# Kernel optimization log

Hardware: AMD Instinct MI355X
Metric: run time of the kernel (lower is better)

Reference implementation:

```python
import jax, jax.numpy as jnp
import numpy as np

NEG_SLOPE = 0.2  # PyG GATConv default leaky_relu slope


def gat_conv(x, src, dst, n, W, a_src, a_dst, bias, concat):
    """PyG-style GATConv (add_self_loops already applied to src/dst)."""
    H, C = a_src.shape
    h = (x @ W).reshape(n, H, C)                      # [N,H,C]
    al_src = jnp.einsum('nhc,hc->nh', h, a_src)       # [N,H]
    al_dst = jnp.einsum('nhc,hc->nh', h, a_dst)       # [N,H]
    e = jax.nn.leaky_relu(al_src[src] + al_dst[dst], NEG_SLOPE)  # [E,H]
    # segment softmax over incoming edges of each dst node
    m = jax.ops.segment_max(e, dst, num_segments=n)   # [N,H]
    ex = jnp.exp(e - m[dst])
    denom = jax.ops.segment_sum(ex, dst, num_segments=n)
    alpha = ex / denom[dst]                            # [E,H]
    out = jax.ops.segment_sum(h[src] * alpha[:, :, None], dst, num_segments=n)  # [N,H,C]
    if concat:
        out = out.reshape(n, H * C)
    else:
        out = out.mean(axis=1)
    return out + bias


def setup_inputs() -> dict:
    key = jax.random.key(0)
    ks = jax.random.split(key, 12)
    N, E = 100000, 1600000
    IN, HID, OUT, H = 128, 16, 32, 4
    x = jax.random.normal(ks[0], (N, IN), dtype=jnp.float32)
    edge_index = jax.random.randint(ks[1], (2, E), 0, N, dtype=jnp.int64)
    s = 0.1
    W1 = jax.random.normal(ks[2], (IN, H * HID), dtype=jnp.float32) * s
    a_src1 = jax.random.normal(ks[3], (H, HID), dtype=jnp.float32) * s
    a_dst1 = jax.random.normal(ks[4], (H, HID), dtype=jnp.float32) * s
    b1 = jnp.zeros((H * HID,), dtype=jnp.float32)
    W2 = jax.random.normal(ks[5], (H * HID, H * OUT), dtype=jnp.float32) * s
    a_src2 = jax.random.normal(ks[6], (H, OUT), dtype=jnp.float32) * s
    a_dst2 = jax.random.normal(ks[7], (H, OUT), dtype=jnp.float32) * s
    b2 = jnp.zeros((OUT,), dtype=jnp.float32)
    return {"x": x, "edge_index": edge_index,
            "W1": W1, "a_src1": a_src1, "a_dst1": a_dst1, "b1": b1,
            "W2": W2, "a_src2": a_src2, "a_dst2": a_dst2, "b2": b2}


def reference(x, edge_index, W1, a_src1, a_dst1, b1, W2, a_src2, a_dst2, b2):
    n = x.shape[0]
    loop = jnp.arange(n, dtype=edge_index.dtype)
    src = jnp.concatenate([edge_index[0], loop])
    dst = jnp.concatenate([edge_index[1], loop])
    # dropout is identity at inference
    h = gat_conv(x, src, dst, n, W1, a_src1, a_dst1, b1, concat=True)
    h = gat_conv(h, src, dst, n, W2, a_src2, a_dst2, b2, concat=False)
    h = jax.nn.elu(h)
    return jax.nn.log_softmax(h, axis=1)
```

## Files before the change

### kernel.cpp

```cpp
#include <hip/hip_runtime.h>
#include <hip/hip_fp16.h>
#include <cstdint>
#include <cstddef>

#define NEG 0.2f
#define TILE 4096
#define WEXP(e) __expf((e) > 0.f ? (e) : NEG * (e))

typedef int i4v __attribute__((ext_vector_type(4)));

__device__ __forceinline__ i4v ld_i4(const int* p) {
    i4v r;
    __builtin_memcpy(&r, p, 16);
    return r;
}
__device__ __forceinline__ __half2 bch(unsigned v) { __half2 r; *(unsigned*)&r = v; return r; }
__device__ __forceinline__ __half2 bchi(int v) { __half2 r; *(int*)&r = v; return r; }


__global__ __launch_bounds__(256) void bhist_k(const int* __restrict__ ei, int* __restrict__ bc, int E, int nbk) {
    __shared__ int sb[256];
    int t = threadIdx.x;
    sb[t] = 0;
    __syncthreads();
    int stride = gridDim.x * 256;
    for (int i = blockIdx.x * 256 + t; i < E; i += stride) {
        int d = __builtin_nontemporal_load(ei + E + i);
        atomicAdd(&sb[d >> 9], 1);
    }
    __syncthreads();
    if (t < nbk && sb[t] > 0) atomicAdd(&bc[t], sb[t]);
}


__global__ __launch_bounds__(256) void bscan_k(const int* __restrict__ bc, int* __restrict__ bb,
                                               int* __restrict__ curA, int nbk) {
    __shared__ int sm[256];
    int t = threadIdx.x;
    int v = (t < nbk) ? bc[t] : 0;
    sm[t] = v; __syncthreads();
    for (int off = 1; off < 256; off <<= 1) {
        int u = (t >= off) ? sm[t - off] : 0;
        __syncthreads();
        sm[t] += u;
        __syncthreads();
    }
    if (t < nbk) {
        int ex = sm[t] - v;
        bb[t] = ex;
        curA[t] = ex;
        if (t == nbk - 1) bb[nbk] = sm[t];
    }
}


__global__ __launch_bounds__(256) void partA_k(const int* __restrict__ ei, int* __restrict__ curA,
                                               uint2* __restrict__ pairs, int E, int nbk) {
    __shared__ int scnt[256];
    __shared__ int sc[256];
    __shared__ int sbase[256];
    __shared__ int gbase[256];
    __shared__ int cur2[256];
    __shared__ int ssrc[TILE];
    __shared__ int sdst[TILE];
    int t = threadIdx.x;
    int ntiles = (E + TILE - 1) / TILE;
    for (int tile = blockIdx.x; tile < ntiles; tile += gridDim.x) {
        int base = tile * TILE;
        int cntE = min(TILE, E - base);
        scnt[t] = 0;
        __syncthreads();
        int mys[16], myd[16];
        #pragma unroll
        for (int j = 0; j < 16; j++) {
            int i = base + t + 256 * j;
            int s = 0, d = -1;
            if (i < E) {
                s = __builtin_nontemporal_load(ei + i);
                d = __builtin_nontemporal_load(ei + E + i);
            }
            mys[j] = s; myd[j] = d;
            if (d >= 0) atomicAdd(&scnt[d >> 9], 1);
        }
        __syncthreads();
        sc[t] = scnt[t];
        __syncthreads();
        for (int off = 1; off < 256; off <<= 1) {
            int u = (t >= off) ? sc[t - off] : 0;
            __syncthreads();
            sc[t] += u;
            __syncthreads();
        }
        int myb = sc[t] - scnt[t];
        sbase[t] = myb;
        cur2[t] = myb;
        if (t < nbk && scnt[t] > 0) gbase[t] = atomicAdd(&curA[t], scnt[t]);
        __syncthreads();
        #pragma unroll
        for (int j = 0; j < 16; j++) {
            int d = myd[j];
            if (d >= 0) {
                int b = d >> 9;
                int pos = atomicAdd(&cur2[b], 1);
                ssrc[pos] = mys[j];
                sdst[pos] = d;
            }
        }
        __syncthreads();
        for (int i = t; i < cntE; i += 256) {
            int d = sdst[i];
            int b = d >> 9;
            int addr = gbase[b] + (i - sbase[b]);
            pairs[addr] = make_uint2((unsigned)ssrc[i], (unsigned)d);
        }
        __syncthreads();
    }
}


__global__ __launch_bounds__(256) void partB2_k(const uint2* __restrict__ pin, const int* __restrict__ bb,
                                                int* __restrict__ rp, int* __restrict__ cnt,
                                                int* __restrict__ srcout, int N) {
    __shared__ int cur[512];
    __shared__ int sc[512];
    int b = blockIdx.x, t = threadIdx.x;
    int d0 = b << 9;
    cur[t] = 0; cur[t + 256] = 0;
    __syncthreads();
    int ebase = bb[b], eend = bb[b + 1];
    for (int j = ebase + t; j < eend; j += 256) {
        int d = (int)pin[j].y;
        atomicAdd(&cur[d - d0], 1);
    }
    __syncthreads();
    sc[t] = cur[t]; sc[t + 256] = cur[t + 256];
    __syncthreads();
    for (int off = 1; off <= 256; off <<= 1) {
        int a0 = (t >= off) ? sc[t - off] : 0;
        int a1 = sc[t + 256 - off];
        __syncthreads();
        sc[t] += a0; sc[t + 256] += a1;
        __syncthreads();
    }
    int base0 = ebase + sc[t] - cur[t];
    int base1 = ebase + sc[t + 256] - cur[t + 256];
    if (d0 + t < N)       { rp[d0 + t] = base0;       cnt[d0 + t] = cur[t]; }
    if (d0 + t + 256 < N) { rp[d0 + t + 256] = base1; cnt[d0 + t + 256] = cur[t + 256]; }
    cur[t] = base0; cur[t + 256] = base1;
    __syncthreads();
    for (int j = ebase + t; j < eend; j += 256) {
        uint2 p = pin[j];
        int d = (int)p.y;
        int pos = atomicAdd(&cur[d - d0], 1);
        srcout[pos] = (int)p.x;
    }
}


__global__ __launch_bounds__(256) void gemm1_k(const float* __restrict__ x, const float* __restrict__ W,
                                               const float* __restrict__ a_src, const float* __restrict__ a_dst,
                                               __half* __restrict__ h, float* __restrict__ alsrc,
                                               float* __restrict__ aldst, int N) {
    __shared__ float Bs[128 * 64];
    __shared__ float xt[64 * 68];
    int t = threadIdx.x;
    for (int i = t; i < 128 * 64 / 4; i += 256)
        ((float4*)Bs)[i] = ((const float4*)W)[i];
    int ct = t & 15, rt = t >> 4;
    int head = ct >> 2, cq = ct & 3;
    float asv[4], adv[4];
    #pragma unroll
    for (int j = 0; j < 4; j++) {
        asv[j] = a_src[head * 16 + 4 * cq + j];
        adv[j] = a_dst[head * 16 + 4 * cq + j];
    }
    int ntiles = (N + 63) >> 6;
    for (int tile = blockIdx.x; tile < ntiles; tile += gridDim.x) {
        int r0 = tile << 6;
        float acc[4][4];
        #pragma unroll
        for (int i = 0; i < 4; i++)
            #pragma unroll
            for (int j = 0; j < 4; j++) acc[i][j] = 0.f;
        for (int kc = 0; kc < 128; kc += 64) {
            __syncthreads();
            int srow = t >> 4, sf4 = t & 15;
            #pragma unroll
            for (int p = 0; p < 4; p++) {
                int r = r0 + srow + 16 * p;
                float4 v = make_float4(0.f, 0.f, 0.f, 0.f);
                if (r < N) v = *(const float4*)(x + (size_t)r * 128 + kc + 4 * sf4);
                int rr = srow + 16 * p, k0 = 4 * sf4;
                int colb = 4 * (((rr >> 2) + sf4) & 15) + (rr & 3);
                xt[(k0 + 0) * 68 + colb] = v.x;
                xt[(k0 + 1) * 68 + colb] = v.y;
                xt[(k0 + 2) * 68 + colb] = v.z;
                xt[(k0 + 3) * 68 + colb] = v.w;
            }
            __syncthreads();
            #pragma unroll 4
            for (int k = 0; k < 64; k++) {
                float4 bv = *(float4*)&Bs[(kc + k) * 64 + 4 * ct];
                float4 xv = *(float4*)&xt[k * 68 + 4 * ((rt + (k >> 2)) & 15)];
                acc[0][0] = fmaf(xv.x, bv.x, acc[0][0]);
                acc[0][1] = fmaf(xv.x, bv.y, acc[0][1]);
                acc[0][2] = fmaf(xv.x, bv.z, acc[0][2]);
                acc[0][3] = fmaf(xv.x, bv.w, acc[0][3]);
                acc[1][0] = fmaf(xv.y, bv.x, acc[1][0]);
                acc[1][1] = fmaf(xv.y, bv.y, acc[1][1]);
                acc[1][2] = fmaf(xv.y, bv.z, acc[1][2]);
                acc[1][3] = fmaf(xv.y, bv.w, acc[1][3]);
                acc[2][0] = fmaf(xv.z, bv.x, acc[2][0]);
                acc[2][1] = fmaf(xv.z, bv.y, acc[2][1]);
                acc[2][2] = fmaf(xv.z, bv.z, acc[2][2]);
                acc[2][3] = fmaf(xv.z, bv.w, acc[2][3]);
                acc[3][0] = fmaf(xv.w, bv.x, acc[3][0]);
                acc[3][1] = fmaf(xv.w, bv.y, acc[3][1]);
                acc[3][2] = fmaf(xv.w, bv.z, acc[3][2]);
                acc[3][3] = fmaf(xv.w, bv.w, acc[3][3]);
            }
        }
        #pragma unroll
        for (int i = 0; i < 4; i++) {
            int r = r0 + 4 * rt + i;
            float ps = 0.f, pd = 0.f;
            #pragma unroll
            for (int j = 0; j < 4; j++) {
                ps = fmaf(acc[i][j], asv[j], ps);
                pd = fmaf(acc[i][j], adv[j], pd);
            }
            ps += __shfl_xor(ps, 1); ps += __shfl_xor(ps, 2);
            pd += __shfl_xor(pd, 1); pd += __shfl_xor(pd, 2);
            if (r < N) {
                __half2 h0 = __floats2half2_rn(acc[i][0], acc[i][1]);
                __half2 h1 = __floats2half2_rn(acc[i][2], acc[i][3]);
                *(__half2*)(h + (size_t)r * 64 + 4 * ct) = h0;
                *(__half2*)(h + (size_t)r * 64 + 4 * ct + 2) = h1;
                if (cq == 0) { alsrc[r * 4 + head] = ps; aldst[r * 4 + head] = pd; }
            }
        }
    }
}


__global__ __launch_bounds__(256) void prew_k(const float* __restrict__ W2, const float* __restrict__ as2,
                                              const float* __restrict__ ad2, float* __restrict__ was,
                                              float* __restrict__ wad, uint2* __restrict__ wkg) {
    int t = threadIdx.x;
    int k = t >> 2, hh = t & 3;
    const float* wrow = W2 + k * 128 + hh * 32;
    const float* av = as2 + hh * 32;
    const float* dv = ad2 + hh * 32;
    float s = 0.f, ds = 0.f;
    #pragma unroll 8
    for (int c = 0; c < 32; c++) {
        float w = wrow[c];
        s = fmaf(w, av[c], s);
        ds = fmaf(w, dv[c], ds);
    }
    was[t] = s;
    wad[t] = ds;
    #pragma unroll
    for (int j = 0; j < 8; j++) {
        int e = t * 8 + j;
        int cp = e >> 7, k2 = e & 127;
        int h = k2 >> 5, kk = (2 * k2) & 63;
        const float* w0 = W2 + kk * 128 + h * 32;
        const float* w1 = W2 + (kk + 1) * 128 + h * 32;
        __half2 hx = __floats2half2_rn(w0[2 * cp], w1[2 * cp]);
        __half2 hy = __floats2half2_rn(w0[2 * cp + 1], w1[2 * cp + 1]);
        uint2 v;
        v.x = *(unsigned*)&hx;
        v.y = *(unsigned*)&hy;
        wkg[e] = v;
    }
}


__global__ __launch_bounds__(256) void node1_k(const __half* __restrict__ h, const int* __restrict__ srccol,
                                               const float* __restrict__ alsrc, const float* __restrict__ aldst,
                                               const int* __restrict__ rp, const int* __restrict__ cnt,
                                               const float* __restrict__ bias,
                                               const float* __restrict__ was, const float* __restrict__ wad,
                                               __half* __restrict__ out,
                                               float* __restrict__ alsrc2, float* __restrict__ aldst2, int N) {
    int t = threadIdx.x;
    int d = (blockIdx.x * 256 + t) >> 4;
    if (d >= N) return;
    int c = t & 15;
    int eh = c >> 2, hh = c & 3;
    int mh = c >> 2;
    const uint2* hb = (const uint2*)h;
    float myad = aldst[d * 4 + hh];
    float selfw = WEXP(alsrc[d * 4 + hh] + myad);
    __half2 sh2 = __float2half2_rn(selfw);
    int si = *(int*)&sh2;
    float mden = (eh == 0) ? selfw : 0.f;
    uint2 u = hb[((size_t)d << 4) + c];
    __half2 smy = bchi(__shfl(si, mh, 16));
    __half2 acc0 = __hmul2(smy, bch(u.x));
    __half2 acc1 = __hmul2(smy, bch(u.y));
    int start = rp[d], deg = cnt[d];
    int nq = deg >> 2;
    int i = 0;
    #define N1_PROC(G0, G1, G2, G3, AW) { \
        float w_ = WEXP((AW) + myad); \
        mden += w_; \
        __half2 wh_ = __float2half2_rn(w_); \
        int wi_ = *(int*)&wh_; \
        __half2 q0_ = bchi(__shfl(wi_, 0 + mh, 16)); \
        __half2 q1_ = bchi(__shfl(wi_, 4 + mh, 16)); \
        __half2 q2_ = bchi(__shfl(wi_, 8 + mh, 16)); \
        __half2 q3_ = bchi(__shfl(wi_, 12 + mh, 16)); \
        acc0 = __hfma2(q0_, bch(G0.x), acc0); acc1 = __hfma2(q0_, bch(G0.y), acc1); \
        acc0 = __hfma2(q1_, bch(G1.x), acc0); acc1 = __hfma2(q1_, bch(G1.y), acc1); \
        acc0 = __hfma2(q2_, bch(G2.x), acc0); acc1 = __hfma2(q2_, bch(G2.y), acc1); \
        acc0 = __hfma2(q3_, bch(G3.x), acc0); acc1 = __hfma2(q3_, bch(G3.y), acc1); }
    if (nq > 0) {
        i4v sv = ld_i4(srccol + start);
        uint2 g0 = hb[((size_t)(unsigned)sv.x << 4) + c];
        uint2 g1 = hb[((size_t)(unsigned)sv.y << 4) + c];
        uint2 g2 = hb[((size_t)(unsigned)sv.z << 4) + c];
        uint2 g3 = hb[((size_t)(unsigned)sv.w << 4) + c];
        int my = (eh == 0) ? sv.x : (eh == 1) ? sv.y : (eh == 2) ? sv.z : sv.w;
        float aw = alsrc[(size_t)my * 4 + hh];
        i4v nv = (nq > 1) ? ld_i4(srccol + start + 4) : sv;
        for (int q = 1; q < nq; q++) {
            uint2 n0 = hb[((size_t)(unsigned)nv.x << 4) + c];
            uint2 n1 = hb[((size_t)(unsigned)nv.y << 4) + c];
            uint2 n2 = hb[((size_t)(unsigned)nv.z << 4) + c];
            uint2 n3 = hb[((size_t)(unsigned)nv.w << 4) + c];
            int nmy = (eh == 0) ? nv.x : (eh == 1) ? nv.y : (eh == 2) ? nv.z : nv.w;
            float naw = alsrc[(size_t)nmy * 4 + hh];
            i4v nv2 = (q + 1 < nq) ? ld_i4(srccol + start + 4 * (q + 1)) : nv;
            N1_PROC(g0, g1, g2, g3, aw)
            g0 = n0; g1 = n1; g2 = n2; g3 = n3; aw = naw; nv = nv2;
        }
        N1_PROC(g0, g1, g2, g3, aw)
        i = nq << 2;
    }
    for (; i < deg; i++) {
        int s = srccol[start + i];
        uint2 us = hb[((size_t)(unsigned)s << 4) + c];
        float w = WEXP(alsrc[(size_t)s * 4 + hh] + myad);
        mden += (eh == 0) ? w : 0.f;
        __half2 wh = __float2half2_rn(w);
        int wi = *(int*)&wh;
        __half2 qq = bchi(__shfl(wi, mh, 16));
        acc0 = __hfma2(qq, bch(us.x), acc0);
        acc1 = __hfma2(qq, bch(us.y), acc1);
    }
    mden += __shfl_xor(mden, 4, 16);
    mden += __shfl_xor(mden, 8, 16);
    float den = __shfl(mden, mh, 16);
    float inv = 1.f / den;
    float2 f0 = __half22float2(acc0), f1 = __half22float2(acc1);
    float4 b = *(const float4*)(bias + 4 * c);
    float v0 = f0.x * inv + b.x, v1 = f0.y * inv + b.y;
    float v2 = f1.x * inv + b.z, v3 = f1.y * inv + b.w;
    __half2 o0 = __floats2half2_rn(v0, v1);
    __half2 o1 = __floats2half2_rn(v2, v3);
    uint2 o; o.x = *(unsigned*)&o0; o.y = *(unsigned*)&o1;
    *(uint2*)(out + (size_t)d * 64 + 4 * c) = o;
    const float4* was4 = (const float4*)was;
    const float4* wad4 = (const float4*)wad;
    float4 wa0 = was4[4 * c + 0], wa1 = was4[4 * c + 1], wa2 = was4[4 * c + 2], wa3 = was4[4 * c + 3];
    float4 wd0 = wad4[4 * c + 0], wd1 = wad4[4 * c + 1], wd2 = wad4[4 * c + 2], wd3 = wad4[4 * c + 3];
    float4 ps, pd;
    ps.x = fmaf(v0, wa0.x, fmaf(v1, wa1.x, fmaf(v2, wa2.x, v3 * wa3.x)));
    ps.y = fmaf(v0, wa0.y, fmaf(v1, wa1.y, fmaf(v2, wa2.y, v3 * wa3.y)));
    ps.z = fmaf(v0, wa0.z, fmaf(v1, wa1.z, fmaf(v2, wa2.z, v3 * wa3.z)));
    ps.w = fmaf(v0, wa0.w, fmaf(v1, wa1.w, fmaf(v2, wa2.w, v3 * wa3.w)));
    pd.x = fmaf(v0, wd0.x, fmaf(v1, wd1.x, fmaf(v2, wd2.x, v3 * wd3.x)));
    pd.y = fmaf(v0, wd0.y, fmaf(v1, wd1.y, fmaf(v2, wd2.y, v3 * wd3.y)));
    pd.z = fmaf(v0, wd0.z, fmaf(v1, wd1.z, fmaf(v2, wd2.z, v3 * wd3.z)));
    pd.w = fmaf(v0, wd0.w, fmaf(v1, wd1.w, fmaf(v2, wd2.w, v3 * wd3.w)));
    #pragma unroll
    for (int off = 1; off <= 8; off <<= 1) {
        ps.x += __shfl_xor(ps.x, off); ps.y += __shfl_xor(ps.y, off);
        ps.z += __shfl_xor(ps.z, off); ps.w += __shfl_xor(ps.w, off);
        pd.x += __shfl_xor(pd.x, off); pd.y += __shfl_xor(pd.y, off);
        pd.z += __shfl_xor(pd.z, off); pd.w += __shfl_xor(pd.w, off);
    }
    if (c == 0) {
        *(float4*)(alsrc2 + (size_t)d * 4) = ps;
        *(float4*)(aldst2 + (size_t)d * 4) = pd;
    }
}


#define EDGE_SH(J, U) { \
    __half2 l_ = bch(U.x), h_ = bch(U.y); \
    __half2 qa = bchi(__shfl(wi, 4 * J + 0, 16)); \
    __half2 qb = bchi(__shfl(wi, 4 * J + 1, 16)); \
    __half2 qc = bchi(__shfl(wi, 4 * J + 2, 16)); \
    __half2 qd = bchi(__shfl(wi, 4 * J + 3, 16)); \
    aA0 = __hfma2(qa, l_, aA0); aA1 = __hfma2(qa, h_, aA1); \
    aB0 = __hfma2(qb, l_, aB0); aB1 = __hfma2(qb, h_, aB1); \
    aC0 = __hfma2(qc, l_, aC0); aC1 = __hfma2(qc, h_, aC1); \
    aD0 = __hfma2(qd, l_, aD0); aD1 = __hfma2(qd, h_, aD1); }

__global__ __launch_bounds__(256) void node2_k(const __half* __restrict__ h1o, const int* __restrict__ srccol,
                                               const float* __restrict__ alsrc, const float* __restrict__ aldst,
                                               const int* __restrict__ rp, const int* __restrict__ cnt,
                                               const uint2* __restrict__ wkg, const float* __restrict__ b2,
                                               float* __restrict__ out, int N) {
    __shared__ unsigned wt[16 * 260];
    __shared__ unsigned ys[16 * 132];
    int t = threadIdx.x;
    #pragma unroll
    for (int j = 0; j < 8; j++) {
        int i = t + 256 * j;
        int cp0 = i >> 7, k20 = i & 127;
        *(uint2*)&wt[cp0 * 260 + 2 * k20] = wkg[i];
    }
    int d = blockIdx.x * 16 + (t >> 4);
    int c = t & 15;
    bool live = d < N;
    __half2 hz = __float2half2_rn(0.f);
    __half2 y00 = hz, y01 = hz, y10 = hz, y11 = hz;
    __half2 y20 = hz, y21 = hz, y30 = hz, y31 = hz;
    if (live) {
        int eh = c >> 2;
        int hh = c & 3;
        const uint2* hb = (const uint2*)h1o;
        float myad = aldst[d * 4 + hh];
        float selfw = WEXP(alsrc[d * 4 + hh] + myad);
        __half2 selfh = __float2half2_rn(selfw);
        int selfi = *(int*)&selfh;
        float mden = (eh == 0) ? selfw : 0.f;
        uint2 u = hb[((size_t)d << 4) + c];
        __half2 lo = bch(u.x), hi = bch(u.y);
        __half2 sA = bchi(__shfl(selfi, 0, 16));
        __half2 sB = bchi(__shfl(selfi, 1, 16));
        __half2 sC = bchi(__shfl(selfi, 2, 16));
        __half2 sD = bchi(__shfl(selfi, 3, 16));
        __half2 aA0 = __hmul2(sA, lo), aA1 = __hmul2(sA, hi);
        __half2 aB0 = __hmul2(sB, lo), aB1 = __hmul2(sB, hi);
        __half2 aC0 = __hmul2(sC, lo), aC1 = __hmul2(sC, hi);
        __half2 aD0 = __hmul2(sD, lo), aD1 = __hmul2(sD, hi);
        int start = rp[d], deg = cnt[d];
        int nq = deg >> 2;
        int i = 0;
        #define N2_PROC(G0, G1, G2, G3, AW) { \
            float w_ = WEXP((AW) + myad); \
            mden += w_; \
            __half2 wh_ = __float2half2_rn(w_); \
            int wi = *(int*)&wh_; \
            EDGE_SH(0, G0) EDGE_SH(1, G1) EDGE_SH(2, G2) EDGE_SH(3, G3) }
        if (nq > 0) {
            i4v sv = ld_i4(srccol + start);
            uint2 g0 = hb[((size_t)(unsigned)sv.x << 4) + c];
            uint2 g1 = hb[((size_t)(unsigned)sv.y << 4) + c];
            uint2 g2 = hb[((size_t)(unsigned)sv.z << 4) + c];
            uint2 g3 = hb[((size_t)(unsigned)sv.w << 4) + c];
            int my = (eh == 0) ? sv.x : (eh == 1) ? sv.y : (eh == 2) ? sv.z : sv.w;
            float aw = alsrc[(size_t)my * 4 + hh];
            i4v nv = (nq > 1) ? ld_i4(srccol + start + 4) : sv;
            for (int q = 1; q < nq; q++) {
                uint2 n0 = hb[((size_t)(unsigned)nv.x << 4) + c];
                uint2 n1 = hb[((size_t)(unsigned)nv.y << 4) + c];
                uint2 n2 = hb[((size_t)(unsigned)nv.z << 4) + c];
                uint2 n3 = hb[((size_t)(unsigned)nv.w << 4) + c];
                int nmy = (eh == 0) ? nv.x : (eh == 1) ? nv.y : (eh == 2) ? nv.z : nv.w;
                float naw = alsrc[(size_t)nmy * 4 + hh];
                i4v nv2 = (q + 1 < nq) ? ld_i4(srccol + start + 4 * (q + 1)) : nv;
                N2_PROC(g0, g1, g2, g3, aw)
                g0 = n0; g1 = n1; g2 = n2; g3 = n3; aw = naw; nv = nv2;
            }
            N2_PROC(g0, g1, g2, g3, aw)
            i = nq << 2;
        }
        for (; i < deg; i++) {
            int s = srccol[start + i];
            uint2 us = hb[((size_t)(unsigned)s << 4) + c];
            float w = WEXP(alsrc[(size_t)s * 4 + hh] + myad);
            mden += (eh == 0) ? w : 0.f;
            __half2 wh = __float2half2_rn(w);
            int wi = *(int*)&wh;
            EDGE_SH(0, us)
        }
        mden += __shfl_xor(mden, 4, 16);
        mden += __shfl_xor(mden, 8, 16);
        float dnA = __shfl(mden, 0, 16);
        float dnB = __shfl(mden, 1, 16);
        float dnC = __shfl(mden, 2, 16);
        float dnD = __shfl(mden, 3, 16);
        __half2 jA = __float2half2_rn(0.25f / dnA), jB = __float2half2_rn(0.25f / dnB);
        __half2 jC = __float2half2_rn(0.25f / dnC), jD = __float2half2_rn(0.25f / dnD);
        y00 = __hmul2(jA, aA0); y01 = __hmul2(jA, aA1);
        y10 = __hmul2(jB, aB0); y11 = __hmul2(jB, aB1);
        y20 = __hmul2(jC, aC0); y21 = __hmul2(jC, aC1);
        y30 = __hmul2(jD, aD0); y31 = __hmul2(jD, aD1);
        unsigned* yp = ys + (t >> 4) * 132 + 2 * c;
        *(uint2*)&yp[0]  = make_uint2(*(unsigned*)&y00, *(unsigned*)&y01);
        *(uint2*)&yp[32] = make_uint2(*(unsigned*)&y10, *(unsigned*)&y11);
        *(uint2*)&yp[64] = make_uint2(*(unsigned*)&y20, *(unsigned*)&y21);
        *(uint2*)&yp[96] = make_uint2(*(unsigned*)&y30, *(unsigned*)&y31);
    }
    __syncthreads();
    if (!live) return;
    int n = t >> 4, cp = c;
    const unsigned* yr = ys + n * 132;
    const unsigned* wr = wt + cp * 260;
    float f0 = 0.f, f1 = 0.f;
    for (int kc = 0; kc < 128; kc += 16) {
        __half2 a0 = hz, a1 = hz;
        #pragma unroll
        for (int j = 0; j < 4; j++) {
            int k2 = kc + 4 * j;
            uint4 yv = *(const uint4*)&yr[k2];
            uint4 w0 = *(const uint4*)&wr[2 * k2];
            uint4 w1 = *(const uint4*)&wr[2 * k2 + 4];
            a0 = __hfma2(bch(yv.x), bch(w0.x), a0); a1 = __hfma2(bch(yv.x), bch(w0.y), a1);
            a0 = __hfma2(bch(yv.y), bch(w0.z), a0); a1 = __hfma2(bch(yv.y), bch(w0.w), a1);
            a0 = __hfma2(bch(yv.z), bch(w1.x), a0); a1 = __hfma2(bch(yv.z), bch(w1.y), a1);
            a0 = __hfma2(bch(yv.w), bch(w1.z), a0); a1 = __hfma2(bch(yv.w), bch(w1.w), a1);
        }
        float2 q0 = __half22float2(a0), q1 = __half22float2(a1);
        f0 += q0.x + q0.y;
        f1 += q1.x + q1.y;
    }
    float e0 = f0 + b2[2 * cp];
    float e1 = f1 + b2[2 * cp + 1];
    e0 = e0 > 0.f ? e0 : __expf(e0) - 1.f;
    e1 = e1 > 0.f ? e1 : __expf(e1) - 1.f;
    float mx = fmaxf(e0, e1);
    #pragma unroll
    for (int off = 1; off <= 8; off <<= 1) mx = fmaxf(mx, __shfl_xor(mx, off, 16));
    float sm = __expf(e0 - mx) + __expf(e1 - mx);
    #pragma unroll
    for (int off = 1; off <= 8; off <<= 1) sm += __shfl_xor(sm, off, 16);
    float ls = mx + __logf(sm);
    float2 ov = make_float2(e0 - ls, e1 - ls);
    *(float2*)(out + (size_t)d * 32 + 2 * cp) = ov;
}


extern "C" void kernel_launch(void* const* d_in, const int* in_sizes, int n_in,
                              void* d_out, int out_size, void* d_ws, size_t ws_size,
                              hipStream_t stream) {
    const float* x   = (const float*)d_in[0];
    const int*   ei  = (const int*)d_in[1];
    const float* W1  = (const float*)d_in[2];
    const float* as1 = (const float*)d_in[3];
    const float* ad1 = (const float*)d_in[4];
    const float* b1  = (const float*)d_in[5];
    const float* W2  = (const float*)d_in[6];
    const float* as2 = (const float*)d_in[7];
    const float* ad2 = (const float*)d_in[8];
    const float* b2  = (const float*)d_in[9];
    float* out = (float*)d_out;
    int N = in_sizes[0] / 128;
    int E = in_sizes[1] / 2;

    char* base = (char*)d_ws;
    size_t off = 0;
    auto alloc = [&](size_t bytes) -> char* {
        char* p = base + off;
        off = (off + bytes + 255) & ~(size_t)255;
        return p;
    };
    __half* h1h   = (__half*)alloc((size_t)N * 64 * 2);
    __half* h1o   = (__half*)alloc((size_t)N * 64 * 2);
    uint2*  pairs = (uint2*)alloc((size_t)E * 8);
    float* alsrc1 = (float*)alloc((size_t)N * 4 * 4);
    float* aldst1 = (float*)alloc((size_t)N * 4 * 4);
    float* alsrc2 = (float*)alloc((size_t)N * 4 * 4);
    float* aldst2 = (float*)alloc((size_t)N * 4 * 4);
    float* was    = (float*)alloc(256 * 4);
    float* wad    = (float*)alloc(256 * 4);
    uint2* wkg    = (uint2*)alloc(2048 * 8);
    int* cnt  = (int*)alloc((size_t)N * 4);
    int* rp   = (int*)alloc((size_t)N * 4);
    int* curA = (int*)alloc(256 * 4);
    int* bc   = (int*)alloc(256 * 4);
    int* bb   = (int*)alloc(260 * 4);
    int* srccol = (int*)alloc((size_t)E * 4);

    int nbk = (N + 511) >> 9;
    int ntilesA = (E + TILE - 1) / TILE;
    int nt1 = (N + 63) >> 6;

    prew_k<<<1, 256, 0, stream>>>(W2, as2, ad2, was, wad, wkg);
    hipMemsetAsync(bc, 0, 256 * 4, stream);
    bhist_k<<<512, 256, 0, stream>>>(ei, bc, E, nbk);
    bscan_k<<<1, 256, 0, stream>>>(bc, bb, curA, nbk);
    partA_k<<<ntilesA, 256, 0, stream>>>(ei, curA, pairs, E, nbk);
    partB2_k<<<nbk, 256, 0, stream>>>(pairs, bb, rp, cnt, srccol, N);

    gemm1_k<<<(nt1 + 1) / 2, 256, 0, stream>>>(x, W1, as1, ad1, h1h, alsrc1, aldst1, N);
    node1_k<<<(N + 15) / 16, 256, 0, stream>>>(h1h, srccol, alsrc1, aldst1, rp, cnt, b1,
                                               was, wad, h1o, alsrc2, aldst2, N);
    node2_k<<<(N + 15) / 16, 256, 0, stream>>>(h1o, srccol, alsrc2, aldst2, rp, cnt,
                                               wkg, b2, out, N);
}
```

Before: 312.3 us.

## Use packed half FMA in layer-1 GEMM and register-block node2 projection

The layer-1 feature GEMM now converts W and x tiles to packed half2 in shared memory and accumulates with __hfma2 in 16-step chunks, flushing to fp32. This halves shared-memory footprint and doubles math throughput per instruction, at the cost of reduced precision in the x@W product. In node2, the output projection now has half the threads each compute two nodes, so each weight load from shared memory is reused across both rows.

```diff
diff --git a/kernel.cpp b/kernel.cpp
--- a/kernel.cpp
+++ b/kernel.cpp
@@ -161,11 +161,14 @@
                                                const float* __restrict__ a_src, const float* __restrict__ a_dst,
                                                __half* __restrict__ h, float* __restrict__ alsrc,
                                                float* __restrict__ aldst, int N) {
-    __shared__ float Bs[128 * 64];
-    __shared__ float xt[64 * 68];
+    __shared__ unsigned wh[64 * 64];
+    __shared__ unsigned xh[64 * 68];
     int t = threadIdx.x;
-    for (int i = t; i < 128 * 64 / 4; i += 256)
-        ((float4*)Bs)[i] = ((const float4*)W)[i];
+    for (int i = t; i < 4096; i += 256) {
+        int k2 = i >> 6, col = i & 63;
+        __half2 hv = __floats2half2_rn(W[(2 * k2) * 64 + col], W[(2 * k2 + 1) * 64 + col]);
+        wh[i] = *(unsigned*)&hv;
+    }
     int ct = t & 15, rt = t >> 4;
     int head = ct >> 2, cq = ct & 3;
     float asv[4], adv[4];
@@ -177,48 +180,55 @@
     int ntiles = (N + 63) >> 6;
     for (int tile = blockIdx.x; tile < ntiles; tile += gridDim.x) {
         int r0 = tile << 6;
+        __syncthreads();
+        #pragma unroll
+        for (int p = 0; p < 8; p++) {
+            int i = t + 256 * p;
+            int f4i = i & 31, row = i >> 5;
+            int r = r0 + row;
+            float4 v = make_float4(0.f, 0.f, 0.f, 0.f);
+            if (r < N) v = *(const float4*)(x + (size_t)r * 128 + 4 * f4i);
+            __half2 p0 = __floats2half2_rn(v.x, v.y);
+            __half2 p1 = __floats2half2_rn(v.z, v.w);
+            xh[(2 * f4i) * 68 + row] = *(unsigned*)&p0;
+            xh[(2 * f4i + 1) * 68 + row] = *(unsigned*)&p1;
+        }
+        __syncthreads();
         float acc[4][4];
         #pragma unroll
         for (int i = 0; i < 4; i++)
             #pragma unroll
             for (int j = 0; j < 4; j++) acc[i][j] = 0.f;
-        for (int kc = 0; kc < 128; kc += 64) {
-            __syncthreads();
-            int srow = t >> 4, sf4 = t & 15;
+        __half2 hz = __float2half2_rn(0.f);
+        for (int kc = 0; kc < 64; kc += 16) {
+            __half2 ah[4][4];
             #pragma unroll
-            for (int p = 0; p < 4; p++) {
-                int r = r0 + srow + 16 * p;
-                float4 v = make_float4(0.f, 0.f, 0.f, 0.f);
-                if (r < N) v = *(const float4*)(x + (size_t)r * 128 + kc + 4 * sf4);
-                int rr = srow + 16 * p, k0 = 4 * sf4;
-                int colb = 4 * (((rr >> 2) + sf4) & 15) + (rr & 3);
-                xt[(k0 + 0) * 68 + colb] = v.x;
-                xt[(k0 + 1) * 68 + colb] = v.y;
-                xt[(k0 + 2) * 68 + colb] = v.z;
-                xt[(k0 + 3) * 68 + colb] = v.w;
+            for (int i = 0; i < 4; i++)
+                #pragma unroll
+                for (int j = 0; j < 4; j++) ah[i][j] = hz;
+            #pragma unroll
+            for (int j = 0; j < 16; j++) {
+                int k2 = kc + j;
+                uint4 wv = *(const uint4*)&wh[k2 * 64 + 4 * ct];
+                uint4 xv = *(const uint4*)&xh[k2 * 68 + 4 * rt];
+                __half2 w0 = bch(wv.x), w1 = bch(wv.y), w2 = bch(wv.z), w3 = bch(wv.w);
+                __half2 x0 = bch(xv.x), x1 = bch(xv.y), x2 = bch(xv.z), x3 = bch(xv.w);
+                ah[0][0] = __hfma2(x0, w0, ah[0][0]); ah[0][1] = __hfma2(x0, w1, ah[0][1]);
+                ah[0][2] = __hfma2(x0, w2, ah[0][2]); ah[0][3] = __hfma2(x0, w3, ah[0][3]);
+                ah[1][0] = __hfma2(x1, w0, ah[1][0]); ah[1][1] = __hfma2(x1, w1, ah[1][1]);
+                ah[1][2] = __hfma2(x1, w2, ah[1][2]); ah[1][3] = __hfma2(x1, w3, ah[1][3]);
+                ah[2][0] = __hfma2(x2, w0, ah[2][0]); ah[2][1] = __hfma2(x2, w1, ah[2][1]);
+                ah[2][2] = __hfma2(x2, w2, ah[2][2]); ah[2][3] = __hfma2(x2, w3, ah[2][3]);
+                ah[3][0] = __hfma2(x3, w0, ah[3][0]); ah[3][1] = __hfma2(x3, w1, ah[3][1]);
+                ah[3][2] = __hfma2(x3, w2, ah[3][2]); ah[3][3] = __hfma2(x3, w3, ah[3][3]);
             }
-            __syncthreads();
-            #pragma unroll 4
-            for (int k = 0; k < 64; k++) {
-                float4 bv = *(float4*)&Bs[(kc + k) * 64 + 4 * ct];
-                float4 xv = *(float4*)&xt[k * 68 + 4 * ((rt + (k >> 2)) & 15)];
-                acc[0][0] = fmaf(xv.x, bv.x, acc[0][0]);
-                acc[0][1] = fmaf(xv.x, bv.y, acc[0][1]);
-                acc[0][2] = fmaf(xv.x, bv.z, acc[0][2]);
-                acc[0][3] = fmaf(xv.x, bv.w, acc[0][3]);
-                acc[1][0] = fmaf(xv.y, bv.x, acc[1][0]);
-                acc[1][1] = fmaf(xv.y, bv.y, acc[1][1]);
-                acc[1][2] = fmaf(xv.y, bv.z, acc[1][2]);
-                acc[1][3] = fmaf(xv.y, bv.w, acc[1][3]);
-                acc[2][0] = fmaf(xv.z, bv.x, acc[2][0]);
-                acc[2][1] = fmaf(xv.z, bv.y, acc[2][1]);
-                acc[2][2] = fmaf(xv.z, bv.z, acc[2][2]);
-                acc[2][3] = fmaf(xv.z, bv.w, acc[2][3]);
-                acc[3][0] = fmaf(xv.w, bv.x, acc[3][0]);
-                acc[3][1] = fmaf(xv.w, bv.y, acc[3][1]);
-                acc[3][2] = fmaf(xv.w, bv.z, acc[3][2]);
-                acc[3][3] = fmaf(xv.w, bv.w, acc[3][3]);
-            }
+            #pragma unroll
+            for (int i = 0; i < 4; i++)
+                #pragma unroll
+                for (int j = 0; j < 4; j++) {
+                    float2 q = __half22float2(ah[i][j]);
+                    acc[i][j] += q.x + q.y;
+                }
         }
         #pragma unroll
         for (int i = 0; i < 4; i++) {
@@ -418,8 +428,6 @@
     int c = t & 15;
     bool live = d < N;
     __half2 hz = __float2half2_rn(0.f);
-    __half2 y00 = hz, y01 = hz, y10 = hz, y11 = hz;
-    __half2 y20 = hz, y21 = hz, y30 = hz, y31 = hz;
     if (live) {
         int eh = c >> 2;
         int hh = c & 3;
@@ -488,10 +496,10 @@
         float dnD = __shfl(mden, 3, 16);
         __half2 jA = __float2half2_rn(0.25f / dnA), jB = __float2half2_rn(0.25f / dnB);
         __half2 jC = __float2half2_rn(0.25f / dnC), jD = __float2half2_rn(0.25f / dnD);
-        y00 = __hmul2(jA, aA0); y01 = __hmul2(jA, aA1);
-        y10 = __hmul2(jB, aB0); y11 = __hmul2(jB, aB1);
-        y20 = __hmul2(jC, aC0); y21 = __hmul2(jC, aC1);
-        y30 = __hmul2(jD, aD0); y31 = __hmul2(jD, aD1);
+        __half2 y00 = __hmul2(jA, aA0), y01 = __hmul2(jA, aA1);
+        __half2 y10 = __hmul2(jB, aB0), y11 = __hmul2(jB, aB1);
+        __half2 y20 = __hmul2(jC, aC0), y21 = __hmul2(jC, aC1);
+        __half2 y30 = __hmul2(jD, aD0), y31 = __hmul2(jD, aD1);
         unsigned* yp = ys + (t >> 4) * 132 + 2 * c;
         *(uint2*)&yp[0]  = make_uint2(*(unsigned*)&y00, *(unsigned*)&y01);
         *(uint2*)&yp[32] = make_uint2(*(unsigned*)&y10, *(unsigned*)&y11);
@@ -499,41 +507,63 @@
         *(uint2*)&yp[96] = make_uint2(*(unsigned*)&y30, *(unsigned*)&y31);
     }
     __syncthreads();
-    if (!live) return;
-    int n = t >> 4, cp = c;
-    const unsigned* yr = ys + n * 132;
+    if (t >= 128) return;
+    int np = t >> 4, cp = t & 15;
+    int d0 = blockIdx.x * 16 + 2 * np;
+    if (d0 >= N) return;
+    bool l1 = (d0 + 1) < N;
+    const unsigned* yr0 = ys + (2 * np) * 132;
+    const unsigned* yr1 = yr0 + 132;
     const unsigned* wr = wt + cp * 260;
-    float f0 = 0.f, f1 = 0.f;
+    float f00 = 0.f, f01 = 0.f, f10 = 0.f, f11 = 0.f;
     for (int kc = 0; kc < 128; kc += 16) {
-        __half2 a0 = hz, a1 = hz;
+        __half2 a00 = hz, a01 = hz, a10 = hz, a11 = hz;
         #pragma unroll
         for (int j = 0; j < 4; j++) {
             int k2 = kc + 4 * j;
-            uint4 yv = *(const uint4*)&yr[k2];
+            uint4 yv0 = *(const uint4*)&yr0[k2];
+            uint4 yv1 = *(const uint4*)&yr1[k2];
             uint4 w0 = *(const uint4*)&wr[2 * k2];
             uint4 w1 = *(const uint4*)&wr[2 * k2 + 4];
-            a0 = __hfma2(bch(yv.x), bch(w0.x), a0); a1 = __hfma2(bch(yv.x), bch(w0.y), a1);
-            a0 = __hfma2(bch(yv.y), bch(w0.z), a0); a1 = __hfma2(bch(yv.y), bch(w0.w), a1);
-            a0 = __hfma2(bch(yv.z), bch(w1.x), a0); a1 = __hfma2(bch(yv.z), bch(w1.y), a1);
-            a0 = __hfma2(bch(yv.w), bch(w1.z), a0); a1 = __hfma2(bch(yv.w), bch(w1.w), a1);
-        }
-        float2 q0 = __half22float2(a0), q1 = __half22float2(a1);
-        f0 += q0.x + q0.y;
-        f1 += q1.x + q1.y;
-    }
-    float e0 = f0 + b2[2 * cp];
-    float e1 = f1 + b2[2 * cp + 1];
-    e0 = e0 > 0.f ? e0 : __expf(e0) - 1.f;
-    e1 = e1 > 0.f ? e1 : __expf(e1) - 1.f;
-    float mx = fmaxf(e0, e1);
+            a00 = __hfma2(bch(yv0.x), bch(w0.x), a00); a01 = __hfma2(bch(yv0.x), bch(w0.y), a01);
+            a00 = __hfma2(bch(yv0.y), bch(w0.z), a00); a01 = __hfma2(bch(yv0.y), bch(w0.w), a01);
+            a00 = __hfma2(bch(yv0.z), bch(w1.x), a00); a01 = __hfma2(bch(yv0.z), bch(w1.y), a01);
+            a00 = __hfma2(bch(yv0.w), bch(w1.z), a00); a01 = __hfma2(bch(yv0.w), bch(w1.w), a01);
+            a10 = __hfma2(bch(yv1.x), bch(w0.x), a10); a11 = __hfma2(bch(yv1.x), bch(w0.y), a11);
+            a10 = __hfma2(bch(yv1.y), bch(w0.z), a10); a11 = __hfma2(bch(yv1.y), bch(w0.w), a11);
+            a10 = __hfma2(bch(yv1.z), bch(w1.x), a10); a11 = __hfma2(bch(yv1.z), bch(w1.y), a11);
+            a10 = __hfma2(bch(yv1.w), bch(w1.z), a10); a11 = __hfma2(bch(yv1.w), bch(w1.w), a11);
+        }
+        float2 q;
+        q = __half22float2(a00); f00 += q.x + q.y;
+        q = __half22float2(a01); f01 += q.x + q.y;
+        q = __half22float2(a10); f10 += q.x + q.y;
+        q = __half22float2(a11); f11 += q.x + q.y;
+    }
+    float b20 = b2[2 * cp], b21 = b2[2 * cp + 1];
+    float e00 = f00 + b20, e01 = f01 + b21;
+    float e10 = f10 + b20, e11 = f11 + b21;
+    e00 = e00 > 0.f ? e00 : __expf(e00) - 1.f;
+    e01 = e01 > 0.f ? e01 : __expf(e01) - 1.f;
+    e10 = e10 > 0.f ? e10 : __expf(e10) - 1.f;
+    e11 = e11 > 0.f ? e11 : __expf(e11) - 1.f;
+    float mx0 = fmaxf(e00, e01), mx1 = fmaxf(e10, e11);
     #pragma unroll
-    for (int off = 1; off <= 8; off <<= 1) mx = fmaxf(mx, __shfl_xor(mx, off, 16));
-    float sm = __expf(e0 - mx) + __expf(e1 - mx);
+    for (int off = 1; off <= 8; off <<= 1) {
+        mx0 = fmaxf(mx0, __shfl_xor(mx0, off, 16));
+        mx1 = fmaxf(mx1, __shfl_xor(mx1, off, 16));
+    }
+    float sm0 = __expf(e00 - mx0) + __expf(e01 - mx0);
+    float sm1 = __expf(e10 - mx1) + __expf(e11 - mx1);
     #pragma unroll
-    for (int off = 1; off <= 8; off <<= 1) sm += __shfl_xor(sm, off, 16);
-    float ls = mx + __logf(sm);
-    float2 ov = make_float2(e0 - ls, e1 - ls);
-    *(float2*)(out + (size_t)d * 32 + 2 * cp) = ov;
+    for (int off = 1; off <= 8; off <<= 1) {
+        sm0 += __shfl_xor(sm0, off, 16);
+        sm1 += __shfl_xor(sm1, off, 16);
+    }
+    float ls0 = mx0 + __logf(sm0);
+    float ls1 = mx1 + __logf(sm1);
+    *(float2*)(out + (size_t)d0 * 32 + 2 * cp) = make_float2(e00 - ls0, e01 - ls0);
+    if (l1) *(float2*)(out + (size_t)(d0 + 1) * 32 + 2 * cp) = make_float2(e10 - ls1, e11 - ls1);
 }
 
 
```

Result: slower. 371.6 us (+19.0%).
